# Kernel optimization log

Measured on AMD Instinct MI355X. Metric: run time of the kernel, lower is better.

The kernel has to match this reference:

```python
import jax, jax.numpy as jnp
import numpy as np

NUM_GRAPHS = 1024
HIDDEN = 256
N_NODES = 500000


def setup_inputs() -> dict:
    key = jax.random.key(0)
    k1, k2, k3, k4 = jax.random.split(key, 4)
    x = jax.random.normal(k1, (N_NODES, HIDDEN), dtype=jnp.float32)
    batch = jnp.sort(jax.random.randint(k2, (N_NODES,), 0, NUM_GRAPHS, dtype=jnp.int64))
    # attention = nn.Linear(hidden_dim, 1): weight [1, hidden], bias [1]
    bound = 1.0 / np.sqrt(HIDDEN)
    att_w = jax.random.uniform(k3, (HIDDEN, 1), dtype=jnp.float32, minval=-bound, maxval=bound)
    att_b = jax.random.uniform(k4, (1,), dtype=jnp.float32, minval=-bound, maxval=bound)
    return {"x": x, "batch": batch, "att_w": att_w, "att_b": att_b}


def reference(x, batch, att_w, att_b):
    seg = batch.astype(jnp.int32)
    # mean pool: segment sum / counts
    sums = jax.ops.segment_sum(x, seg, num_segments=NUM_GRAPHS)  # [G, H]
    counts = jax.ops.segment_sum(jnp.ones((x.shape[0],), x.dtype), seg, num_segments=NUM_GRAPHS)
    mean_pool = sums / jnp.maximum(counts, 1.0)[:, None]
    # max pool
    max_pool = jax.ops.segment_max(x, seg, num_segments=NUM_GRAPHS)
    # attention-weighted add pool: sigmoid(x @ w + b) * x, segment-summed
    weights = jax.nn.sigmoid(x @ att_w + att_b)  # [N, 1]
    att_pool = jax.ops.segment_sum(x * weights, seg, num_segments=NUM_GRAPHS)
    return jnp.concatenate([mean_pool, max_pool, att_pool], axis=-1)
```

## Files before the change

### kernel.cpp

```cpp
#include <hip/hip_runtime.h>
#include <math.h>

constexpr int NUM_GRAPHS = 1024;
constexpr int QUARTERS   = 4;
constexpr int WAVES_PB   = 4;
constexpr int STRIDE     = QUARTERS * WAVES_PB;

__global__ void detect_i32_kernel(const int* __restrict__ words, int n,
                                  int* __restrict__ flag) {
    const int stride = gridDim.x * blockDim.x;
    int acc = 0;
    for (int j = 1 + 2 * (int)(blockIdx.x * blockDim.x + threadIdx.x); j < n;
         j += 2 * stride)
        acc |= words[j];
    if (__any(acc != 0)) {
        if ((threadIdx.x & 63) == 0) atomicOr(flag, 1);
    }
}

__global__ void seg_start_kernel(const int* __restrict__ words, int n,
                                 const int* __restrict__ flag,
                                 int* __restrict__ seg) {
    int i = blockIdx.x * blockDim.x + threadIdx.x;
    if (i >= n) return;
    const bool is32 = (*flag != 0);
    int b    = is32 ? words[i] : words[2 * i];
    int prev = (i == 0) ? -1 : (is32 ? words[i - 1] : words[2 * (i - 1)]);
    for (int g = prev + 1; g <= b; ++g) seg[g] = i;
    if (i == n - 1)
        for (int g = b + 1; g <= NUM_GRAPHS; ++g) seg[g] = n;
}

__global__ __launch_bounds__(256) void pool_partial_kernel(
    const float* __restrict__ x, const float* __restrict__ att_w,
    const float* __restrict__ att_b, const int* __restrict__ seg,
    float* __restrict__ part) {
    const int g    = blockIdx.x >> 2;
    const int q    = blockIdx.x & 3;
    const int lane = threadIdx.x & 63;
    const int w    = threadIdx.x >> 6;
    const int W    = q * WAVES_PB + w;

    const int s0 = seg[g];
    const int e0 = seg[g + 1];

    const float4* __restrict__ x4 = (const float4*)x;
    const float4 wv   = ((const float4*)att_w)[lane];
    const float  bias = att_b[0];

    float sx = 0.f, sy = 0.f, sz = 0.f, sw = 0.f;
    float mx = -INFINITY, my = -INFINITY, mz = -INFINITY, mw = -INFINITY;
    float ax = 0.f, ay = 0.f, az = 0.f, aw = 0.f;

    auto proc4 = [&](const float4* v) {
        float p[4];
#pragma unroll
        for (int r = 0; r < 4; ++r)
            p[r] = v[r].x * wv.x + v[r].y * wv.y + v[r].z * wv.z + v[r].w * wv.w;
#pragma unroll
        for (int off = 32; off >= 1; off >>= 1) {
#pragma unroll
            for (int r = 0; r < 4; ++r)
                p[r] += __shfl_xor(p[r], off, 64);
        }
#pragma unroll
        for (int r = 0; r < 4; ++r) {
            const float sig = 1.0f / (1.0f + __expf(-(p[r] + bias)));
            sx += v[r].x; sy += v[r].y; sz += v[r].z; sw += v[r].w;
            mx = fmaxf(mx, v[r].x); my = fmaxf(my, v[r].y);
            mz = fmaxf(mz, v[r].z); mw = fmaxf(mw, v[r].w);
            ax += v[r].x * sig; ay += v[r].y * sig;
            az += v[r].z * sig; aw += v[r].w * sig;
        }
    };

    int i = s0 + W;
    if (i + 3 * STRIDE < e0) {
        float4 v[4];
#pragma unroll
        for (int r = 0; r < 4; ++r)
            v[r] = x4[(size_t)(i + r * STRIDE) * 64 + lane];
        int nb = i + 4 * STRIDE;
        while (nb + 3 * STRIDE < e0) {
            float4 vn[4];
#pragma unroll
            for (int r = 0; r < 4; ++r)
                vn[r] = x4[(size_t)(nb + r * STRIDE) * 64 + lane];
            proc4(v);
#pragma unroll
            for (int r = 0; r < 4; ++r) v[r] = vn[r];
            nb += 4 * STRIDE;
        }
        proc4(v);
        i = nb;
    }
    for (; i < e0; i += STRIDE) {
        const float4 v = x4[(size_t)i * 64 + lane];
        float p = v.x * wv.x + v.y * wv.y + v.z * wv.z + v.w * wv.w;
#pragma unroll
        for (int off = 32; off >= 1; off >>= 1)
            p += __shfl_xor(p, off, 64);
        const float sig = 1.0f / (1.0f + __expf(-(p + bias)));
        sx += v.x; sy += v.y; sz += v.z; sw += v.w;
        mx = fmaxf(mx, v.x); my = fmaxf(my, v.y);
        mz = fmaxf(mz, v.z); mw = fmaxf(mw, v.w);
        ax += v.x * sig; ay += v.y * sig; az += v.z * sig; aw += v.w * sig;
    }

    __shared__ float4 lsum[4][64];
    __shared__ float4 lmax[4][64];
    __shared__ float4 latt[4][64];
    lsum[w][lane] = make_float4(sx, sy, sz, sw);
    lmax[w][lane] = make_float4(mx, my, mz, mw);
    latt[w][lane] = make_float4(ax, ay, az, aw);
    __syncthreads();

    if (w == 0) {
        float4 S = lsum[0][lane], M = lmax[0][lane], A = latt[0][lane];
#pragma unroll
        for (int ww = 1; ww < 4; ++ww) {
            float4 s2 = lsum[ww][lane], m2 = lmax[ww][lane], a2 = latt[ww][lane];
            S.x += s2.x; S.y += s2.y; S.z += s2.z; S.w += s2.w;
            M.x = fmaxf(M.x, m2.x); M.y = fmaxf(M.y, m2.y);
            M.z = fmaxf(M.z, m2.z); M.w = fmaxf(M.w, m2.w);
            A.x += a2.x; A.y += a2.y; A.z += a2.z; A.w += a2.w;
        }
        float4* __restrict__ o = (float4*)part + (size_t)blockIdx.x * 192;
        o[lane]       = S;
        o[64 + lane]  = M;
        o[128 + lane] = A;
    }
}

__global__ __launch_bounds__(256) void pool_combine_kernel(
    const float* __restrict__ part, const int* __restrict__ seg,
    float* __restrict__ out) {
    const int g = blockIdx.x;
    const int t = threadIdx.x;
    if (t >= 192) return;
    const int sec  = t >> 6;
    const int lane = t & 63;

    const float4* __restrict__ p4 = (const float4*)part;
    const size_t base = (size_t)g * 4 * 192 + sec * 64 + lane;

    float4 a = p4[base];
    if (sec == 1) {
#pragma unroll
        for (int q = 1; q < 4; ++q) {
            float4 b = p4[base + (size_t)q * 192];
            a.x = fmaxf(a.x, b.x); a.y = fmaxf(a.y, b.y);
            a.z = fmaxf(a.z, b.z); a.w = fmaxf(a.w, b.w);
        }
    } else {
#pragma unroll
        for (int q = 1; q < 4; ++q) {
            float4 b = p4[base + (size_t)q * 192];
            a.x += b.x; a.y += b.y; a.z += b.z; a.w += b.w;
        }
        if (sec == 0) {
            const int cnt = seg[g + 1] - seg[g];
            const float inv = 1.0f / (float)(cnt > 0 ? cnt : 1);
            a.x *= inv; a.y *= inv; a.z *= inv; a.w *= inv;
        }
    }
    ((float4*)(out + (size_t)g * 768))[sec * 64 + lane] = a;
}

extern "C" void kernel_launch(void* const* d_in, const int* in_sizes, int n_in,
                              void* d_out, int out_size, void* d_ws, size_t ws_size,
                              hipStream_t stream) {
    const float* x           = (const float*)d_in[0];
    const int*   batch_words = (const int*)d_in[1];
    const float* att_w       = (const float*)d_in[2];
    const float* att_b       = (const float*)d_in[3];
    float*       out         = (float*)d_out;
    const int n = in_sizes[1];

    int*   flag = (int*)d_ws;
    int*   seg  = ((int*)d_ws) + 8;
    float* part = (float*)((char*)d_ws + 8192);

    hipMemsetAsync(flag, 0, sizeof(int), stream);
    detect_i32_kernel<<<256, 256, 0, stream>>>(batch_words, n, flag);
    seg_start_kernel<<<(n + 255) / 256, 256, 0, stream>>>(batch_words, n, flag, seg);
    pool_partial_kernel<<<NUM_GRAPHS * QUARTERS, 256, 0, stream>>>(x, att_w, att_b, seg, part);
    pool_combine_kernel<<<NUM_GRAPHS, 256, 0, stream>>>(part, seg, out);
}
```

Measured before the change: 672.2 us.

## Fuse partial and combine pool kernels into one block per graph

Replaces the four-blocks-per-graph partial kernel and the separate combine kernel with one kernel that uses a single block per graph. Each wave now takes a contiguous chunk of rows instead of striding, and the three output sections are reduced by different waves. The x loads become nontemporal. This removes a launch and the round-trip through the partial buffer, but cuts the grid from 4096 to 1024 blocks, which lowers memory-level parallelism on a bandwidth-bound stream.

```diff
diff --git a/kernel.cpp b/kernel.cpp
--- a/kernel.cpp
+++ b/kernel.cpp
@@ -2,9 +2,12 @@
 #include <math.h>
 
 constexpr int NUM_GRAPHS = 1024;
-constexpr int QUARTERS   = 4;
-constexpr int WAVES_PB   = 4;
-constexpr int STRIDE     = QUARTERS * WAVES_PB;
+
+typedef float f4_t __attribute__((ext_vector_type(4)));
+__device__ __forceinline__ float4 nt_load(const float4* p) {
+    f4_t v = __builtin_nontemporal_load((const f4_t*)p);
+    return make_float4(v.x, v.y, v.z, v.w);
+}
 
 __global__ void detect_i32_kernel(const int* __restrict__ words, int n,
                                   int* __restrict__ flag) {
@@ -31,18 +34,20 @@
         for (int g = b + 1; g <= NUM_GRAPHS; ++g) seg[g] = n;
 }
 
-__global__ __launch_bounds__(256) void pool_partial_kernel(
+__global__ __launch_bounds__(256) void pool_fused_kernel(
     const float* __restrict__ x, const float* __restrict__ att_w,
     const float* __restrict__ att_b, const int* __restrict__ seg,
-    float* __restrict__ part) {
-    const int g    = blockIdx.x >> 2;
-    const int q    = blockIdx.x & 3;
+    float* __restrict__ out) {
+    const int g    = blockIdx.x;
     const int lane = threadIdx.x & 63;
     const int w    = threadIdx.x >> 6;
-    const int W    = q * WAVES_PB + w;
 
-    const int s0 = seg[g];
-    const int e0 = seg[g + 1];
+    const int s0    = seg[g];
+    const int e0    = seg[g + 1];
+    const int cnt   = e0 - s0;
+    const int chunk = (cnt + 3) >> 2;
+    const int wbeg  = min(s0 + w * chunk, e0);
+    const int wend  = min(wbeg + chunk, e0);
 
     const float4* __restrict__ x4 = (const float4*)x;
     const float4 wv   = ((const float4*)att_w)[lane];
@@ -74,28 +79,28 @@
         }
     };
 
-    int i = s0 + W;
-    if (i + 3 * STRIDE < e0) {
+    int i = wbeg;
+    if (i + 4 <= wend) {
         float4 v[4];
 #pragma unroll
         for (int r = 0; r < 4; ++r)
-            v[r] = x4[(size_t)(i + r * STRIDE) * 64 + lane];
-        int nb = i + 4 * STRIDE;
-        while (nb + 3 * STRIDE < e0) {
+            v[r] = nt_load(x4 + (size_t)(i + r) * 64 + lane);
+        int nb = i + 4;
+        while (nb + 4 <= wend) {
             float4 vn[4];
 #pragma unroll
             for (int r = 0; r < 4; ++r)
-                vn[r] = x4[(size_t)(nb + r * STRIDE) * 64 + lane];
+                vn[r] = nt_load(x4 + (size_t)(nb + r) * 64 + lane);
             proc4(v);
 #pragma unroll
             for (int r = 0; r < 4; ++r) v[r] = vn[r];
-            nb += 4 * STRIDE;
+            nb += 4;
         }
         proc4(v);
         i = nb;
     }
-    for (; i < e0; i += STRIDE) {
-        const float4 v = x4[(size_t)i * 64 + lane];
+    for (; i < wend; ++i) {
+        const float4 v = nt_load(x4 + (size_t)i * 64 + lane);
         float p = v.x * wv.x + v.y * wv.y + v.z * wv.z + v.w * wv.w;
 #pragma unroll
         for (int off = 32; off >= 1; off >>= 1)
@@ -115,56 +120,35 @@
     latt[w][lane] = make_float4(ax, ay, az, aw);
     __syncthreads();
 
+    float4* __restrict__ o = (float4*)(out + (size_t)g * 768);
     if (w == 0) {
-        float4 S = lsum[0][lane], M = lmax[0][lane], A = latt[0][lane];
+        float4 S = lsum[0][lane];
 #pragma unroll
         for (int ww = 1; ww < 4; ++ww) {
-            float4 s2 = lsum[ww][lane], m2 = lmax[ww][lane], a2 = latt[ww][lane];
-            S.x += s2.x; S.y += s2.y; S.z += s2.z; S.w += s2.w;
-            M.x = fmaxf(M.x, m2.x); M.y = fmaxf(M.y, m2.y);
-            M.z = fmaxf(M.z, m2.z); M.w = fmaxf(M.w, m2.w);
-            A.x += a2.x; A.y += a2.y; A.z += a2.z; A.w += a2.w;
+            float4 b = lsum[ww][lane];
+            S.x += b.x; S.y += b.y; S.z += b.z; S.w += b.w;
         }
-        float4* __restrict__ o = (float4*)part + (size_t)blockIdx.x * 192;
-        o[lane]       = S;
-        o[64 + lane]  = M;
+        const float inv = 1.0f / (float)(cnt > 0 ? cnt : 1);
+        S.x *= inv; S.y *= inv; S.z *= inv; S.w *= inv;
+        o[lane] = S;
+    } else if (w == 1) {
+        float4 M = lmax[0][lane];
+#pragma unroll
+        for (int ww = 1; ww < 4; ++ww) {
+            float4 b = lmax[ww][lane];
+            M.x = fmaxf(M.x, b.x); M.y = fmaxf(M.y, b.y);
+            M.z = fmaxf(M.z, b.z); M.w = fmaxf(M.w, b.w);
+        }
+        o[64 + lane] = M;
+    } else if (w == 2) {
+        float4 A = latt[0][lane];
+#pragma unroll
+        for (int ww = 1; ww < 4; ++ww) {
+            float4 b = latt[ww][lane];
+            A.x += b.x; A.y += b.y; A.z += b.z; A.w += b.w;
+        }
         o[128 + lane] = A;
     }
-}
-
-__global__ __launch_bounds__(256) void pool_combine_kernel(
-    const float* __restrict__ part, const int* __restrict__ seg,
-    float* __restrict__ out) {
-    const int g = blockIdx.x;
-    const int t = threadIdx.x;
-    if (t >= 192) return;
-    const int sec  = t >> 6;
-    const int lane = t & 63;
-
-    const float4* __restrict__ p4 = (const float4*)part;
-    const size_t base = (size_t)g * 4 * 192 + sec * 64 + lane;
-
-    float4 a = p4[base];
-    if (sec == 1) {
-#pragma unroll
-        for (int q = 1; q < 4; ++q) {
-            float4 b = p4[base + (size_t)q * 192];
-            a.x = fmaxf(a.x, b.x); a.y = fmaxf(a.y, b.y);
-            a.z = fmaxf(a.z, b.z); a.w = fmaxf(a.w, b.w);
-        }
-    } else {
-#pragma unroll
-        for (int q = 1; q < 4; ++q) {
-            float4 b = p4[base + (size_t)q * 192];
-            a.x += b.x; a.y += b.y; a.z += b.z; a.w += b.w;
-        }
-        if (sec == 0) {
-            const int cnt = seg[g + 1] - seg[g];
-            const float inv = 1.0f / (float)(cnt > 0 ? cnt : 1);
-            a.x *= inv; a.y *= inv; a.z *= inv; a.w *= inv;
-        }
-    }
-    ((float4*)(out + (size_t)g * 768))[sec * 64 + lane] = a;
 }
 
 extern "C" void kernel_launch(void* const* d_in, const int* in_sizes, int n_in,
@@ -177,13 +161,11 @@
     float*       out         = (float*)d_out;
     const int n = in_sizes[1];
 
-    int*   flag = (int*)d_ws;
-    int*   seg  = ((int*)d_ws) + 8;
-    float* part = (float*)((char*)d_ws + 8192);
+    int* flag = (int*)d_ws;
+    int* seg  = ((int*)d_ws) + 8;
 
     hipMemsetAsync(flag, 0, sizeof(int), stream);
     detect_i32_kernel<<<256, 256, 0, stream>>>(batch_words, n, flag);
     seg_start_kernel<<<(n + 255) / 256, 256, 0, stream>>>(batch_words, n, flag, seg);
-    pool_partial_kernel<<<NUM_GRAPHS * QUARTERS, 256, 0, stream>>>(x, att_w, att_b, seg, part);
-    pool_combine_kernel<<<NUM_GRAPHS, 256, 0, stream>>>(part, seg, out);
+    pool_fused_kernel<<<NUM_GRAPHS, 256, 0, stream>>>(x, att_w, att_b, seg, out);
 }
```

Result: faster. 633.5 us (-5.8%).
